# Performance work log

Measured on AMD Instinct MI355X. Metric: run time of the kernel, lower is better.

Reference implementation:

```python
import jax, jax.numpy as jnp
import numpy as np

B = 131072
EPS = 1e-5

def _attn(x, Wq, Wk, Wv, Wo):
    # x: (B, 10, 1); Wq/Wk/Wv: (1, 16); Wo: (16, 1)
    Q = x @ Wq  # (B, 10, 16)
    K = x @ Wk
    V = x @ Wv
    A = jnp.einsum('bqd,bkd->bqk', Q, K) / 4.0  # sqrt(16) = 4
    A = jax.nn.softmax(A, axis=1)  # NOTE: torch Softmax(dim=1) -> axis 1, not -1
    out = jnp.einsum('bqk,bkd->bqd', A, V) @ Wo  # (B, 10, 1)
    return out[..., 0]  # squeeze -> (B, 10)

def _bn(h, gamma, beta):
    # BatchNorm1d training-mode math (batch stats, biased variance)
    mu = jnp.mean(h, axis=0)
    var = jnp.mean(jnp.square(h - mu), axis=0)
    return gamma * (h - mu) * jax.lax.rsqrt(var + EPS) + beta

def setup_inputs() -> dict:
    key = jax.random.key(0)
    ks = jax.random.split(key, 24)
    n = lambda k, shp, s=1.0: (jax.random.normal(k, shp, dtype=jnp.float32) * s)
    inp = {
        'x':   n(ks[0], (B, 10, 1)),
        'Wq1': n(ks[1], (1, 16)), 'Wk1': n(ks[2], (1, 16)),
        'Wv1': n(ks[3], (1, 16)), 'Wo1': n(ks[4], (16, 1)),
        'Wq2': n(ks[5], (1, 16)), 'Wk2': n(ks[6], (1, 16)),
        'Wv2': n(ks[7], (1, 16)), 'Wo2': n(ks[8], (16, 1)),
        # layer1: Linear(10,128) BN ReLU Linear(128,256) BN ReLU Linear(256,10)
        'W1a': n(ks[9], (10, 128), 0.3), 'b1a': jnp.zeros((128,), jnp.float32),
        'g1a': jnp.ones((128,), jnp.float32), 'be1a': jnp.zeros((128,), jnp.float32),
        'W1b': n(ks[10], (128, 256), 0.09), 'b1b': jnp.zeros((256,), jnp.float32),
        'g1b': jnp.ones((256,), jnp.float32), 'be1b': jnp.zeros((256,), jnp.float32),
        'W1c': n(ks[11], (256, 10), 0.06), 'b1c': jnp.zeros((10,), jnp.float32),
        # layer2: Linear(10,128) BN ReLU Linear(128,256) BN ReLU Linear(256,2)
        'W2a': n(ks[12], (10, 128), 0.3), 'b2a': jnp.zeros((128,), jnp.float32),
        'g2a': jnp.ones((128,), jnp.float32), 'be2a': jnp.zeros((128,), jnp.float32),
        'W2b': n(ks[13], (128, 256), 0.09), 'b2b': jnp.zeros((256,), jnp.float32),
        'g2b': jnp.ones((256,), jnp.float32), 'be2b': jnp.zeros((256,), jnp.float32),
        'W2c': n(ks[14], (256, 2), 0.06), 'b2c': jnp.zeros((2,), jnp.float32),
    }
    return inp

def reference(x, Wq1, Wk1, Wv1, Wo1, Wq2, Wk2, Wv2, Wo2,
              W1a, b1a, g1a, be1a, W1b, b1b, g1b, be1b, W1c, b1c,
              W2a, b2a, g2a, be2a, W2b, b2b, g2b, be2b, W2c, b2c):
    h = _attn(x, Wq1, Wk1, Wv1, Wo1)                 # (B, 10)
    h = jax.nn.relu(_bn(h @ W1a + b1a, g1a, be1a))   # (B, 128)
    h = jax.nn.relu(_bn(h @ W1b + b1b, g1b, be1b))   # (B, 256)
    h = h @ W1c + b1c                                # (B, 10)
    h = _attn(h[..., None], Wq2, Wk2, Wv2, Wo2)      # (B, 10)
    h = jax.nn.relu(_bn(h @ W2a + b2a, g2a, be2a))   # (B, 128)
    h = jax.nn.relu(_bn(h @ W2b + b2b, g2b, be2b))   # (B, 256)
    return h @ W2c + b2c                             # (B, 2)
```

## Files before the change

### kernel.cpp

```cpp
#include <hip/hip_runtime.h>
#include <hip/hip_bf16.h>

#define EPS 1e-5f
constexpr int BN = 131072;
constexpr int NBKT = 32;

typedef __attribute__((ext_vector_type(8))) short bf16x8;
typedef __attribute__((ext_vector_type(4))) float f32x4;

constexpr size_t OFF_H   = 0;
constexpr size_t OFF_HH  = OFF_H  + (size_t)BN*10;
constexpr size_t OFF_M1  = OFF_HH + (size_t)BN*10;
constexpr size_t OFF_S2  = OFF_M1 + 65;
constexpr size_t OFF_M3  = OFF_S2 + 512;
constexpr size_t OFF_S4  = OFF_M3 + 65;
constexpr size_t OFF_WA1 = OFF_S4 + 512;
constexpr size_t OFF_BA1 = OFF_WA1 + 1280;
constexpr size_t OFF_WA2 = OFF_BA1 + 128;
constexpr size_t OFF_BA2 = OFF_WA2 + 1280;
constexpr size_t OFF_SC2 = OFF_BA2 + 128;
constexpr size_t OFF_TC2 = OFF_SC2 + 256;
constexpr size_t OFF_SC4 = OFF_TC2 + 256;
constexpr size_t OFF_TC4 = OFF_SC4 + 256;
constexpr size_t OFF_WB1 = OFF_TC4 + 256;
constexpr size_t OFF_BB1 = OFF_WB1 + 32768;
constexpr size_t OFF_WB2 = OFF_BB1 + 256;
constexpr size_t OFF_BB2 = OFF_WB2 + 32768;
constexpr size_t OFF_P1  = OFF_BB2 + 256;
constexpr size_t OFF_P3  = OFF_P1 + 1024*65;
constexpr size_t OFF_S2B = OFF_P3 + 1024*65;
constexpr size_t OFF_S4B = OFF_S2B + (size_t)NBKT*512;
constexpr size_t OFF_WT1 = OFF_S4B + (size_t)NBKT*512;
constexpr size_t OFF_WT2 = OFF_WT1 + 16384;
constexpr size_t OFF_END = OFF_WT2 + 16384;
constexpr size_t OFF_Z_BYTES = ((OFF_END*4 + 255) & ~(size_t)255);
constexpr size_t WS_NEED = OFF_Z_BYTES + (size_t)256*BN*2;

__device__ __forceinline__ float wsum(float v){
  v += __shfl_down(v, 32);
  v += __shfl_down(v, 16);
  v += __shfl_down(v, 8);
  v += __shfl_down(v, 4);
  v += __shfl_down(v, 2);
  v += __shfl_down(v, 1);
  return v;
}

__device__ __forceinline__ unsigned pk_bf16(float a, float b){
  union { __hip_bfloat16 h[2]; unsigned u; } cv;
  cv.h[0] = __float2bfloat16(a);
  cv.h[1] = __float2bfloat16(b);
  return cv.u;
}

__device__ __forceinline__ unsigned short bf16_1(float a){
  union { __hip_bfloat16 h; unsigned short u; } cv;
  cv.h = __float2bfloat16(a);
  return cv.u;
}

__device__ __forceinline__ void attn10(const float* xr, float cqk, float cvo, float* y){
  #pragma unroll
  for (int q=0;q<10;q++) y[q] = 0.f;
  #pragma unroll
  for (int k=0;k<10;k++){
    float t = cqk * xr[k];
    float m = t*xr[0];
    #pragma unroll
    for (int q=1;q<10;q++) m = fmaxf(m, t*xr[q]);
    float ex[10]; float s = 0.f;
    #pragma unroll
    for (int q=0;q<10;q++){ ex[q] = __expf(t*xr[q]-m); s += ex[q]; }
    float f = xr[k]/s;
    #pragma unroll
    for (int q=0;q<10;q++) y[q] += ex[q]*f;
  }
  #pragma unroll
  for (int q=0;q<10;q++) y[q] *= cvo;
}

__device__ __forceinline__ void moments_block(const float* y, float (*red)[65],
                                              float* Pb, int t, float scale){
  int lane = t & 63, w = t >> 6;
  #pragma unroll
  for (int i=0;i<10;i++){
    float v = wsum(y[i]);
    if (lane==0) red[w][i] = v;
  }
  #pragma unroll
  for (int i=0;i<10;i++){
    #pragma unroll
    for (int j=i;j<10;j++){
      float v = wsum(y[i]*y[j]);
      if (lane==0) red[w][10 + 10*i - i*(i-1)/2 + (j-i)] = v;
    }
  }
  __syncthreads();
  if (t < 65)
    Pb[(size_t)blockIdx.x*65 + t] = (red[0][t]+red[1][t]+red[2][t]+red[3][t])*scale;
}

__device__ __forceinline__ void moments10(const float* y, float* M, int lane){
  #pragma unroll
  for (int i=0;i<10;i++){
    float s = wsum(y[i]);
    if (lane==0) atomicAdd(&M[i], s);
  }
  #pragma unroll
  for (int i=0;i<10;i++){
    #pragma unroll
    for (int j=i;j<10;j++){
      int id = 10*i - i*(i-1)/2 + (j-i);
      float s = wsum(y[i]*y[j]);
      if (lane==0) atomicAdd(&M[10+id], s);
    }
  }
}

__global__ __launch_bounds__(256) void k_attn_in(
    const float* __restrict__ x,
    const float* __restrict__ Wq, const float* __restrict__ Wk,
    const float* __restrict__ Wv, const float* __restrict__ Wo,
    float* __restrict__ h, float* __restrict__ Pb){
  __shared__ float xs[256][11];
  __shared__ float red[4][65];
  int t = threadIdx.x;
  size_t base = (size_t)blockIdx.x*2560;
  for (int idx=t; idx<2560; idx+=256) xs[idx/10][idx%10] = x[base+idx];
  float cqk=0.f, cvo=0.f;
  #pragma unroll
  for (int d=0;d<16;d++){ cqk += Wq[d]*Wk[d]; cvo += Wv[d]*Wo[d]; }
  cqk *= 0.25f;
  __syncthreads();
  float xr[10];
  #pragma unroll
  for (int q=0;q<10;q++) xr[q] = xs[t][q];
  float y[10];
  attn10(xr, cqk, cvo, y);
  #pragma unroll
  for (int q=0;q<10;q++) xs[t][q] = y[q];
  moments_block(y, red, Pb, t, 1.0f);
  for (int idx=t; idx<2560; idx+=256) h[base+idx] = xs[idx/10][idx%10];
}

__global__ void k_fold10_part(const float* __restrict__ Pb, int npart,
                              const float* __restrict__ W,
                              const float* __restrict__ bv, const float* __restrict__ g,
                              const float* __restrict__ be,
                              float* __restrict__ WT, float* __restrict__ bo){
  __shared__ float part[65][8];
  __shared__ float sM[65];
  int t = threadIdx.x;
  if (t < 520){
    int c = t>>3, k = t&7;
    int n = npart>>3;
    float acc = 0.f;
    #pragma unroll 4
    for (int i=0;i<n;i++) acc += Pb[(size_t)(k*n+i)*65 + c];
    part[c][k] = acc;
  }
  __syncthreads();
  if (t < 65){
    float a = 0.f;
    #pragma unroll
    for (int k=0;k<8;k++) a += part[t][k];
    sM[t] = a;
  }
  __syncthreads();
  int j = t;
  if (j >= 128) return;
  const float invB = 1.f/(float)BN;
  float Eh[10];
  #pragma unroll
  for (int i=0;i<10;i++) Eh[i] = sM[i]*invB;
  float wj[10];
  #pragma unroll
  for (int i=0;i<10;i++) wj[i] = W[i*128+j];
  float mu = bv[j];
  #pragma unroll
  for (int i=0;i<10;i++) mu += Eh[i]*wj[i];
  float var = 0.f;
  #pragma unroll
  for (int i=0;i<10;i++){
    #pragma unroll
    for (int l=0;l<10;l++){
      int a = i<l ? i : l, c = i<l ? l : i;
      int id = 10*a - a*(a-1)/2 + (c-a);
      float cov = sM[10+id]*invB - Eh[i]*Eh[l];
      var += wj[i]*wj[l]*cov;
    }
  }
  float s = g[j]*rsqrtf(var + EPS);
  #pragma unroll
  for (int i=0;i<10;i++) WT[j*10+i] = wj[i]*s;
  bo[j] = (bv[j]-mu)*s + be[j];
}

__global__ void k_fold10_atomic(const float* __restrict__ M,
                                const float* __restrict__ W,
                                const float* __restrict__ bv, const float* __restrict__ g,
                                const float* __restrict__ be,
                                float* __restrict__ WT, float* __restrict__ bo){
  int j = threadIdx.x;
  if (j >= 128) return;
  const float invB = 1.f/(float)BN;
  float Eh[10];
  #pragma unroll
  for (int i=0;i<10;i++) Eh[i] = M[i]*invB;
  float wj[10];
  #pragma unroll
  for (int i=0;i<10;i++) wj[i] = W[i*128+j];
  float mu = bv[j];
  #pragma unroll
  for (int i=0;i<10;i++) mu += Eh[i]*wj[i];
  float var = 0.f;
  #pragma unroll
  for (int i=0;i<10;i++){
    #pragma unroll
    for (int l=0;l<10;l++){
      int a = i<l ? i : l, c = i<l ? l : i;
      int id = 10*a - a*(a-1)/2 + (c-a);
      float cov = M[10+id]*invB - Eh[i]*Eh[l];
      var += wj[i]*wj[l]*cov;
    }
  }
  float s = g[j]*rsqrtf(var + EPS);
  #pragma unroll
  for (int i=0;i<10;i++) WT[j*10+i] = wj[i]*s;
  bo[j] = (bv[j]-mu)*s + be[j];
}

__global__ void k_fold_affine(const float* __restrict__ stats,
                              const float* __restrict__ g,
                              const float* __restrict__ be,
                              float* __restrict__ s, float* __restrict__ tt){
  int j = threadIdx.x;
  if (j >= 256) return;
  float su = 0.f, sq = 0.f;
  #pragma unroll 4
  for (int k=0;k<NBKT;k++){
    su += stats[k*512 + j];
    sq += stats[k*512 + 256 + j];
  }
  const float invB = 1.f/(float)BN;
  float mu  = su*invB;
  float var = sq*invB - mu*mu;
  float sc = g[j]*rsqrtf(var + EPS);
  s[j]  = sc;
  tt[j] = be[j] - mu*sc;
}

__global__ __launch_bounds__(256) void k_prep_wt2(
    const float* __restrict__ W1, const float* __restrict__ W2,
    unsigned short* __restrict__ WT1, unsigned short* __restrict__ WT2){
  int g = blockIdx.x;
  const float* W = (g < 128) ? W1 : W2;
  unsigned short* WT = (g < 128) ? WT1 : WT2;
  int idx = (g & 127)*256 + threadIdx.x;
  int c = idx >> 7, k = idx & 127;
  WT[idx] = bf16_1(W[k*256 + c]);
}

__global__ __launch_bounds__(256) void k_layer_mfma(
    const float* __restrict__ h,
    const float* __restrict__ WaT,
    const float* __restrict__ ba,
    const unsigned short* __restrict__ WT,
    const float* __restrict__ bb,
    unsigned short* __restrict__ zt,
    float* __restrict__ stats)
{
  __shared__ unsigned short zs[256*72];
  __shared__ float hs[64][11];
  __shared__ float sWaT[1280];
  __shared__ float sstats[512];
  unsigned short* h1s = zs;
  int t = threadIdx.x;
  int lane = t & 63, w = t >> 6;
  int ci = lane & 15, g = lane >> 4;
  size_t row0 = (size_t)blockIdx.x * 64;

  bf16x8 bfr[4][4];
  #pragma unroll
  for (int nt=0; nt<4; nt++)
    #pragma unroll
    for (int kt=0; kt<4; kt++){
      union { uint4 u; bf16x8 v; } cv;
      cv.u = *(const uint4*)(WT + (size_t)(w*64 + nt*16 + ci)*128 + kt*32 + g*8);
      bfr[nt][kt] = cv.v;
    }

  for (int idx = t; idx < 640; idx += 256) hs[idx/10][idx%10] = h[row0*10 + idx];
  for (int idx = t; idx < 1280; idx += 256) sWaT[idx] = WaT[idx];
  __syncthreads();

  {
    int r = lane;
    int i0 = w * 32;
    float hr[10];
    #pragma unroll
    for (int l=0;l<10;l++) hr[l] = hs[r][l];
    #pragma unroll
    for (int j=0;j<4;j++){
      unsigned pk[4];
      #pragma unroll
      for (int q=0;q<4;q++){
        int i = i0 + j*8 + q*2;
        float v0 = ba[i], v1 = ba[i+1];
        #pragma unroll
        for (int l=0;l<10;l++){
          v0 = fmaf(hr[l], sWaT[i*10+l],     v0);
          v1 = fmaf(hr[l], sWaT[(i+1)*10+l], v1);
        }
        pk[q] = pk_bf16(fmaxf(v0,0.f), fmaxf(v1,0.f));
      }
      int byte = r*256 + (((i0 + j*8)*2) ^ ((r&7)<<4));
      *(uint4*)((char*)h1s + byte) = make_uint4(pk[0],pk[1],pk[2],pk[3]);
    }
  }
  __syncthreads();

  f32x4 acc[4][4];
  #pragma unroll
  for (int mt=0;mt<4;mt++)
    #pragma unroll
    for (int nt=0;nt<4;nt++)
      acc[mt][nt] = (f32x4){0.f,0.f,0.f,0.f};

  #pragma unroll
  for (int mt=0; mt<4; mt++){
    int r = mt*16 + ci;
    bf16x8 af[4];
    #pragma unroll
    for (int kt=0; kt<4; kt++){
      int byte = r*256 + ((kt*64 + g*16) ^ ((r&7)<<4));
      af[kt] = *(const bf16x8*)((const char*)h1s + byte);
    }
    #pragma unroll
    for (int nt=0; nt<4; nt++)
      #pragma unroll
      for (int kt=0; kt<4; kt++)
        acc[mt][nt] = __builtin_amdgcn_mfma_f32_16x16x32_bf16(
            af[kt], bfr[nt][kt], acc[mt][nt], 0, 0, 0);
  }

  float bbv[4];
  #pragma unroll
  for (int nt=0;nt<4;nt++) bbv[nt] = bb[w*64 + nt*16 + ci];
  float csum[4] = {0,0,0,0}, csq[4] = {0,0,0,0};
  #pragma unroll
  for (int mt=0; mt<4; mt++)
    #pragma unroll
    for (int nt=0; nt<4; nt++)
      #pragma unroll
      for (int j=0;j<4;j++){
        float zv = acc[mt][nt][j] + bbv[nt];
        acc[mt][nt][j] = zv;
        csum[nt] += zv;
        csq[nt]  += zv*zv;
      }
  #pragma unroll
  for (int nt=0; nt<4; nt++){
    float s1 = csum[nt], s2 = csq[nt];
    s1 += __shfl_down(s1, 32); s1 += __shfl_down(s1, 16);
    s2 += __shfl_down(s2, 32); s2 += __shfl_down(s2, 16);
    if (lane < 16){
      sstats[w*64 + nt*16 + ci]       = s1;
      sstats[256 + w*64 + nt*16 + ci] = s2;
    }
  }
  __syncthreads();
  int bkt = blockIdx.x & (NBKT-1);
  atomicAdd(&stats[bkt*512 + t], sstats[t]);
  atomicAdd(&stats[bkt*512 + 256 + t], sstats[256+t]);

  #pragma unroll
  for (int mt=0; mt<4; mt++)
    #pragma unroll
    for (int nt=0; nt<4; nt++){
      int c = w*64 + nt*16 + ci;
      int r0 = mt*16 + g*4;
      uint2 v;
      v.x = pk_bf16(acc[mt][nt][0], acc[mt][nt][1]);
      v.y = pk_bf16(acc[mt][nt][2], acc[mt][nt][3]);
      *(uint2*)&zs[c*72 + r0] = v;
    }
  __syncthreads();

  #pragma unroll
  for (int pass=0; pass<8; pass++){
    int c  = (t>>3) + pass*32;
    int rc = (t&7)*8;
    uint4 v = *(const uint4*)&zs[c*72 + rc];
    *(uint4*)(zt + (size_t)c*BN + row0 + rc) = v;
  }
}

__global__ __launch_bounds__(256) void k_consume_mid(
    const unsigned short* __restrict__ zt,
    const float* __restrict__ s_g, const float* __restrict__ t_g,
    const float* __restrict__ Wc,  const float* __restrict__ bc,
    const float* __restrict__ Wq, const float* __restrict__ Wk,
    const float* __restrict__ Wv, const float* __restrict__ Wo,
    float* __restrict__ hh, float* __restrict__ Pb){
  __shared__ float sW[2560];
  __shared__ float ss[256], st[256];
  __shared__ float red[4][65];
  __shared__ float hhs[128][11];
  int t = threadIdx.x;
  for (int idx=t; idx<2560; idx+=256) sW[idx] = Wc[idx];
  ss[t] = s_g[t]; st[t] = t_g[t];
  __syncthreads();
  int r = t >> 1, p = t & 1;
  size_t b = (size_t)blockIdx.x*128 + r;
  float z3[10];
  #pragma unroll
  for (int l=0;l<10;l++) z3[l] = p ? 0.f : bc[l];
  int c0 = p*128;
  #pragma unroll 4
  for (int c=c0; c<c0+128; c++){
    unsigned short u = zt[(size_t)c*BN + b];
    float f = __uint_as_float(((unsigned)u) << 16);
    float h2 = fmaxf(fmaf(ss[c], f, st[c]), 0.f);
    #pragma unroll
    for (int l=0;l<10;l++) z3[l] = fmaf(h2, sW[c*10+l], z3[l]);
  }
  #pragma unroll
  for (int l=0;l<10;l++) z3[l] += __shfl_xor(z3[l], 1);
  float cqk=0.f, cvo=0.f;
  #pragma unroll
  for (int d=0;d<16;d++){ cqk += Wq[d]*Wk[d]; cvo += Wv[d]*Wo[d]; }
  cqk *= 0.25f;
  float y[10];
  attn10(z3, cqk, cvo, y);
  if (!p){
    #pragma unroll
    for (int q=0;q<10;q++) hhs[r][q] = y[q];
  }
  moments_block(y, red, Pb, t, 0.5f);
  for (int idx=t; idx<1280; idx+=256)
    hh[(size_t)blockIdx.x*1280 + idx] = hhs[idx/10][idx%10];
}

__global__ __launch_bounds__(256) void k_consume_out(
    const unsigned short* __restrict__ zt,
    const float* __restrict__ s_g, const float* __restrict__ t_g,
    const float* __restrict__ Wc,  const float* __restrict__ bc,
    float* __restrict__ out){
  __shared__ float sW0[256], sW1[256], ss[256], st[256];
  int t = threadIdx.x;
  sW0[t] = Wc[t*2]; sW1[t] = Wc[t*2+1];
  ss[t] = s_g[t]; st[t] = t_g[t];
  __syncthreads();
  int r = t >> 1, p = t & 1;
  size_t b = (size_t)blockIdx.x*128 + r;
  float o0 = p ? 0.f : bc[0];
  float o1 = p ? 0.f : bc[1];
  int c0 = p*128;
  #pragma unroll 4
  for (int c=c0; c<c0+128; c++){
    unsigned short u = zt[(size_t)c*BN + b];
    float f = __uint_as_float(((unsigned)u) << 16);
    float h5 = fmaxf(fmaf(ss[c], f, st[c]), 0.f);
    o0 = fmaf(h5, sW0[c], o0);
    o1 = fmaf(h5, sW1[c], o1);
  }
  o0 += __shfl_xor(o0, 1);
  o1 += __shfl_xor(o1, 1);
  out[b*2 + p] = p ? o1 : o0;
}

__global__ void k_fold_big(const float* __restrict__ stats,
                           const float* __restrict__ W,
                           const float* __restrict__ bv, const float* __restrict__ g,
                           const float* __restrict__ be,
                           float* __restrict__ Wf, float* __restrict__ bf){
  int j = blockIdx.x*256 + threadIdx.x;
  if (j >= 256) return;
  const float invB = 1.f/(float)BN;
  float mu  = stats[j]*invB;
  float var = stats[256+j]*invB - mu*mu;
  float s = g[j]*rsqrtf(var + EPS);
  bf[j] = (bv[j]-mu)*s + be[j];
  for (int i=0;i<128;i++) Wf[i*256+j] = W[i*256+j]*s;
}

__global__ __launch_bounds__(256) void k_mid(
    const float* __restrict__ h,
    const float* __restrict__ WaT, const float* __restrict__ ba,
    const float* __restrict__ Wb,  const float* __restrict__ bb,
    float* __restrict__ stats){
  int b = blockIdx.x*256 + threadIdx.x;
  if (b >= BN) return;
  float hr[10];
  #pragma unroll
  for (int l=0;l<10;l++) hr[l] = h[(size_t)b*10+l];
  int lane = threadIdx.x & 63;
  for (int jc=0;jc<4;jc++){
    float acc[64];
    #pragma unroll
    for (int j=0;j<64;j++) acc[j] = bb[jc*64+j];
    for (int i=0;i<128;i++){
      float h1 = ba[i];
      #pragma unroll
      for (int l=0;l<10;l++) h1 += hr[l]*WaT[i*10+l];
      h1 = fmaxf(h1, 0.f);
      const float* __restrict__ w = &Wb[i*256 + jc*64];
      #pragma unroll
      for (int j=0;j<64;j++) acc[j] += h1*w[j];
    }
    #pragma unroll
    for (int j=0;j<64;j++){
      float s1 = wsum(acc[j]);
      float s2 = wsum(acc[j]*acc[j]);
      if (lane==0){
        atomicAdd(&stats[jc*64+j], s1);
        atomicAdd(&stats[256+jc*64+j], s2);
      }
    }
  }
}

__global__ __launch_bounds__(256) void k_mid2(
    const float* __restrict__ h,
    const float* __restrict__ WaT, const float* __restrict__ ba,
    const float* __restrict__ Wbf, const float* __restrict__ bbf,
    const float* __restrict__ Wc,  const float* __restrict__ bc,
    const float* __restrict__ Wq, const float* __restrict__ Wk,
    const float* __restrict__ Wv, const float* __restrict__ Wo,
    float* __restrict__ hh, float* __restrict__ M){
  int b = blockIdx.x*256 + threadIdx.x;
  if (b >= BN) return;
  float hr[10];
  #pragma unroll
  for (int l=0;l<10;l++) hr[l] = h[(size_t)b*10+l];
  float z3[10];
  #pragma unroll
  for (int l=0;l<10;l++) z3[l] = bc[l];
  for (int jc=0;jc<4;jc++){
    float acc[64];
    #pragma unroll
    for (int j=0;j<64;j++) acc[j] = bbf[jc*64+j];
    for (int i=0;i<128;i++){
      float h1 = ba[i];
      #pragma unroll
      for (int l=0;l<10;l++) h1 += hr[l]*WaT[i*10+l];
      h1 = fmaxf(h1, 0.f);
      const float* __restrict__ w = &Wbf[i*256 + jc*64];
      #pragma unroll
      for (int j=0;j<64;j++) acc[j] += h1*w[j];
    }
    #pragma unroll
    for (int j=0;j<64;j++){
      float h2 = fmaxf(acc[j], 0.f);
      const float* __restrict__ wc = &Wc[(jc*64+j)*10];
      #pragma unroll
      for (int l=0;l<10;l++) z3[l] += h2*wc[l];
    }
  }
  float cqk=0.f, cvo=0.f;
  #pragma unroll
  for (int d=0;d<16;d++){ cqk += Wq[d]*Wk[d]; cvo += Wv[d]*Wo[d]; }
  cqk *= 0.25f;
  float y[10];
  attn10(z3, cqk, cvo, y);
  #pragma unroll
  for (int q=0;q<10;q++) hh[(size_t)b*10+q] = y[q];
  moments10(y, M, threadIdx.x & 63);
}

__global__ __launch_bounds__(256) void k_out(
    const float* __restrict__ h,
    const float* __restrict__ WaT, const float* __restrict__ ba,
    const float* __restrict__ Wbf, const float* __restrict__ bbf,
    const float* __restrict__ Wc,  const float* __restrict__ bc,
    float* __restrict__ out){
  int b = blockIdx.x*256 + threadIdx.x;
  if (b >= BN) return;
  float hr[10];
  #pragma unroll
  for (int l=0;l<10;l++) hr[l] = h[(size_t)b*10+l];
  float o0 = bc[0], o1 = bc[1];
  for (int jc=0;jc<4;jc++){
    float acc[64];
    #pragma unroll
    for (int j=0;j<64;j++) acc[j] = bbf[jc*64+j];
    for (int i=0;i<128;i++){
      float h4 = ba[i];
      #pragma unroll
      for (int l=0;l<10;l++) h4 += hr[l]*WaT[i*10+l];
      h4 = fmaxf(h4, 0.f);
      const float* __restrict__ w = &Wbf[i*256 + jc*64];
      #pragma unroll
      for (int j=0;j<64;j++) acc[j] += h4*w[j];
    }
    #pragma unroll
    for (int j=0;j<64;j++){
      float h5 = fmaxf(acc[j], 0.f);
      o0 += h5*Wc[(jc*64+j)*2];
      o1 += h5*Wc[(jc*64+j)*2+1];
    }
  }
  out[(size_t)b*2]   = o0;
  out[(size_t)b*2+1] = o1;
}

extern "C" void kernel_launch(void* const* d_in, const int* in_sizes, int n_in,
                              void* d_out, int out_size, void* d_ws, size_t ws_size,
                              hipStream_t stream){
  const float* x   = (const float*)d_in[0];
  const float* Wq1 = (const float*)d_in[1];
  const float* Wk1 = (const float*)d_in[2];
  const float* Wv1 = (const float*)d_in[3];
  const float* Wo1 = (const float*)d_in[4];
  const float* Wq2 = (const float*)d_in[5];
  const float* Wk2 = (const float*)d_in[6];
  const float* Wv2 = (const float*)d_in[7];
  const float* Wo2 = (const float*)d_in[8];
  const float* W1a = (const float*)d_in[9];  const float* b1a = (const float*)d_in[10];
  const float* g1a = (const float*)d_in[11]; const float* be1a= (const float*)d_in[12];
  const float* W1b = (const float*)d_in[13]; const float* b1b = (const float*)d_in[14];
  const float* g1b = (const float*)d_in[15]; const float* be1b= (const float*)d_in[16];
  const float* W1c = (const float*)d_in[17]; const float* b1c = (const float*)d_in[18];
  const float* W2a = (const float*)d_in[19]; const float* b2a = (const float*)d_in[20];
  const float* g2a = (const float*)d_in[21]; const float* be2a= (const float*)d_in[22];
  const float* W2b = (const float*)d_in[23]; const float* b2b = (const float*)d_in[24];
  const float* g2b = (const float*)d_in[25]; const float* be2b= (const float*)d_in[26];
  const float* W2c = (const float*)d_in[27]; const float* b2c = (const float*)d_in[28];

  float* f   = (float*)d_ws;
  float* h   = f + OFF_H;
  float* hh  = f + OFF_HH;
  float* M1  = f + OFF_M1;
  float* S2  = f + OFF_S2;
  float* M3  = f + OFF_M3;
  float* S4  = f + OFF_S4;
  float* WA1 = f + OFF_WA1; float* BA1 = f + OFF_BA1;
  float* WA2 = f + OFF_WA2; float* BA2 = f + OFF_BA2;
  float* SC2 = f + OFF_SC2; float* TC2 = f + OFF_TC2;
  float* SC4 = f + OFF_SC4; float* TC4 = f + OFF_TC4;
  float* WB1 = f + OFF_WB1; float* BB1 = f + OFF_BB1;
  float* WB2 = f + OFF_WB2; float* BB2 = f + OFF_BB2;
  float* P1  = f + OFF_P1;  float* P3  = f + OFF_P3;
  float* S2B = f + OFF_S2B; float* S4B = f + OFF_S4B;
  unsigned short* WT1 = (unsigned short*)(f + OFF_WT1);
  unsigned short* WT2 = (unsigned short*)(f + OFF_WT2);
  unsigned short* ZT = (unsigned short*)((char*)d_ws + OFF_Z_BYTES);

  dim3 blk(256);
  dim3 grid256(BN/256);
  dim3 grid128(BN/128);
  dim3 grid64(BN/64);

  if (ws_size >= WS_NEED){
    hipMemsetAsync(S2B, 0, (size_t)2*NBKT*512*sizeof(float), stream);
    k_prep_wt2<<<256,blk,0,stream>>>(W1b, W2b, WT1, WT2);
    k_attn_in<<<grid256,blk,0,stream>>>(x, Wq1,Wk1,Wv1,Wo1, h, P1);
    k_fold10_part<<<1,576,0,stream>>>(P1, 512, W1a,b1a,g1a,be1a, WA1,BA1);
    k_layer_mfma<<<grid64,blk,0,stream>>>(h, WA1,BA1, WT1,b1b, ZT, S2B);
    k_fold_affine<<<1,256,0,stream>>>(S2B, g1b, be1b, SC2, TC2);
    k_consume_mid<<<grid128,blk,0,stream>>>(ZT, SC2,TC2, W1c,b1c,
                                            Wq2,Wk2,Wv2,Wo2, hh, P3);
    k_fold10_part<<<1,576,0,stream>>>(P3, 1024, W2a,b2a,g2a,be2a, WA2,BA2);
    k_layer_mfma<<<grid64,blk,0,stream>>>(hh, WA2,BA2, WT2,b2b, ZT, S4B);
    k_fold_affine<<<1,256,0,stream>>>(S4B, g2b, be2b, SC4, TC4);
    k_consume_out<<<grid128,blk,0,stream>>>(ZT, SC4,TC4, W2c,b2c, (float*)d_out);
  } else {
    hipMemsetAsync(M1, 0, (65+512+65+512)*sizeof(float), stream);
    k_attn_in<<<grid256,blk,0,stream>>>(x, Wq1,Wk1,Wv1,Wo1, h, P1);
    k_fold10_part<<<1,576,0,stream>>>(P1, 512, W1a,b1a,g1a,be1a, WA1,BA1);
    k_mid<<<grid256,blk,0,stream>>>(h, WA1,BA1, W1b,b1b, S2);
    k_fold_big<<<1,256,0,stream>>>(S2, W1b,b1b,g1b,be1b, WB1,BB1);
    k_mid2<<<grid256,blk,0,stream>>>(h, WA1,BA1, WB1,BB1, W1c,b1c,
                                     Wq2,Wk2,Wv2,Wo2, hh, M3);
    k_fold10_atomic<<<1,128,0,stream>>>(M3, W2a,b2a,g2a,be2a, WA2,BA2);
    k_mid<<<grid256,blk,0,stream>>>(hh, WA2,BA2, W2b,b2b, S4);
    k_fold_big<<<1,256,0,stream>>>(S4, W2b,b2b,g2b,be2b, WB2,BB2);
    k_out<<<grid256,blk,0,stream>>>(hh, WA2,BA2, WB2,BB2, W2c,b2c, (float*)d_out);
  }
}
```

Measured before the change: 228.9 us.

## Stage transposed bf16 activations through LDS with wide loads in consumer kernels

The two consumer kernels now process 256 rows per block with one thread per row, instead of two threads per row splitting the channels. Each block stages 64-channel chunks of the column-major bf16 activation buffer into shared memory using 16-byte vector loads, then reads them per thread. This replaces the narrow 2-byte strided global loads and the cross-lane shuffle reduction. The block count halves, the partial-moment count passed to the fold kernel changes from 1024 to 512, and the 0.5 scale factor is dropped. The extra syncthreads per chunk and 32KB of LDS may reduce occupancy.

```diff
diff --git a/kernel.cpp b/kernel.cpp
--- a/kernel.cpp
+++ b/kernel.cpp
@@ -80,7 +80,7 @@
 }
 
 __device__ __forceinline__ void moments_block(const float* y, float (*red)[65],
-                                              float* Pb, int t, float scale){
+                                              float* Pb, int t){
   int lane = t & 63, w = t >> 6;
   #pragma unroll
   for (int i=0;i<10;i++){
@@ -97,7 +97,7 @@
   }
   __syncthreads();
   if (t < 65)
-    Pb[(size_t)blockIdx.x*65 + t] = (red[0][t]+red[1][t]+red[2][t]+red[3][t])*scale;
+    Pb[(size_t)blockIdx.x*65 + t] = red[0][t]+red[1][t]+red[2][t]+red[3][t];
 }
 
 __device__ __forceinline__ void moments10(const float* y, float* M, int lane){
@@ -139,7 +139,7 @@
   attn10(xr, cqk, cvo, y);
   #pragma unroll
   for (int q=0;q<10;q++) xs[t][q] = y[q];
-  moments_block(y, red, Pb, t, 1.0f);
+  moments_block(y, red, Pb, t);
   for (int idx=t; idx<2560; idx+=256) h[base+idx] = xs[idx/10][idx%10];
 }
 
@@ -403,43 +403,53 @@
     const float* __restrict__ Wq, const float* __restrict__ Wk,
     const float* __restrict__ Wv, const float* __restrict__ Wo,
     float* __restrict__ hh, float* __restrict__ Pb){
+  __shared__ __align__(16) unsigned short zs[64*256];
   __shared__ float sW[2560];
   __shared__ float ss[256], st[256];
   __shared__ float red[4][65];
-  __shared__ float hhs[128][11];
   int t = threadIdx.x;
   for (int idx=t; idx<2560; idx+=256) sW[idx] = Wc[idx];
   ss[t] = s_g[t]; st[t] = t_g[t];
-  __syncthreads();
-  int r = t >> 1, p = t & 1;
-  size_t b = (size_t)blockIdx.x*128 + r;
+  size_t b0 = (size_t)blockIdx.x*256;
+
   float z3[10];
   #pragma unroll
-  for (int l=0;l<10;l++) z3[l] = p ? 0.f : bc[l];
-  int c0 = p*128;
-  #pragma unroll 4
-  for (int c=c0; c<c0+128; c++){
-    unsigned short u = zt[(size_t)c*BN + b];
-    float f = __uint_as_float(((unsigned)u) << 16);
-    float h2 = fmaxf(fmaf(ss[c], f, st[c]), 0.f);
-    #pragma unroll
-    for (int l=0;l<10;l++) z3[l] = fmaf(h2, sW[c*10+l], z3[l]);
-  }
-  #pragma unroll
-  for (int l=0;l<10;l++) z3[l] += __shfl_xor(z3[l], 1);
+  for (int l=0;l<10;l++) z3[l] = bc[l];
+
+  int lane32 = t & 31, cl8 = t >> 5;
+  for (int cc=0; cc<4; cc++){
+    __syncthreads();
+    #pragma unroll
+    for (int pass=0; pass<8; pass++){
+      int c_local = pass*8 + cl8;
+      int c = cc*64 + c_local;
+      uint4 v = *(const uint4*)(zt + (size_t)c*BN + b0 + lane32*8);
+      *(uint4*)&zs[c_local*256 + lane32*8] = v;
+    }
+    __syncthreads();
+    #pragma unroll 8
+    for (int c_local=0; c_local<64; c_local++){
+      int c = cc*64 + c_local;
+      float f = __uint_as_float(((unsigned)zs[c_local*256 + t]) << 16);
+      float h2 = fmaxf(fmaf(ss[c], f, st[c]), 0.f);
+      #pragma unroll
+      for (int l=0;l<10;l++) z3[l] = fmaf(h2, sW[c*10+l], z3[l]);
+    }
+  }
+
   float cqk=0.f, cvo=0.f;
   #pragma unroll
   for (int d=0;d<16;d++){ cqk += Wq[d]*Wk[d]; cvo += Wv[d]*Wo[d]; }
   cqk *= 0.25f;
   float y[10];
   attn10(z3, cqk, cvo, y);
-  if (!p){
-    #pragma unroll
-    for (int q=0;q<10;q++) hhs[r][q] = y[q];
-  }
-  moments_block(y, red, Pb, t, 0.5f);
-  for (int idx=t; idx<1280; idx+=256)
-    hh[(size_t)blockIdx.x*1280 + idx] = hhs[idx/10][idx%10];
+  __syncthreads();
+  float* hhs = (float*)zs;
+  #pragma unroll
+  for (int q=0;q<10;q++) hhs[t*10+q] = y[q];
+  moments_block(y, red, Pb, t);
+  for (int idx=t; idx<2560; idx+=256)
+    hh[b0*10 + idx] = hhs[idx];
 }
 
 __global__ __launch_bounds__(256) void k_consume_out(
@@ -447,27 +457,34 @@
     const float* __restrict__ s_g, const float* __restrict__ t_g,
     const float* __restrict__ Wc,  const float* __restrict__ bc,
     float* __restrict__ out){
+  __shared__ __align__(16) unsigned short zs[64*256];
   __shared__ float sW0[256], sW1[256], ss[256], st[256];
   int t = threadIdx.x;
   sW0[t] = Wc[t*2]; sW1[t] = Wc[t*2+1];
   ss[t] = s_g[t]; st[t] = t_g[t];
-  __syncthreads();
-  int r = t >> 1, p = t & 1;
-  size_t b = (size_t)blockIdx.x*128 + r;
-  float o0 = p ? 0.f : bc[0];
-  float o1 = p ? 0.f : bc[1];
-  int c0 = p*128;
-  #pragma unroll 4
-  for (int c=c0; c<c0+128; c++){
-    unsigned short u = zt[(size_t)c*BN + b];
-    float f = __uint_as_float(((unsigned)u) << 16);
-    float h5 = fmaxf(fmaf(ss[c], f, st[c]), 0.f);
-    o0 = fmaf(h5, sW0[c], o0);
-    o1 = fmaf(h5, sW1[c], o1);
-  }
-  o0 += __shfl_xor(o0, 1);
-  o1 += __shfl_xor(o1, 1);
-  out[b*2 + p] = p ? o1 : o0;
+  size_t b0 = (size_t)blockIdx.x*256;
+  float o0 = bc[0], o1 = bc[1];
+  int lane32 = t & 31, cl8 = t >> 5;
+  for (int cc=0; cc<4; cc++){
+    __syncthreads();
+    #pragma unroll
+    for (int pass=0; pass<8; pass++){
+      int c_local = pass*8 + cl8;
+      int c = cc*64 + c_local;
+      uint4 v = *(const uint4*)(zt + (size_t)c*BN + b0 + lane32*8);
+      *(uint4*)&zs[c_local*256 + lane32*8] = v;
+    }
+    __syncthreads();
+    #pragma unroll 8
+    for (int c_local=0; c_local<64; c_local++){
+      int c = cc*64 + c_local;
+      float f = __uint_as_float(((unsigned)zs[c_local*256 + t]) << 16);
+      float h5 = fmaxf(fmaf(ss[c], f, st[c]), 0.f);
+      o0 = fmaf(h5, sW0[c], o0);
+      o1 = fmaf(h5, sW1[c], o1);
+    }
+  }
+  *(float2*)(out + (b0 + t)*2) = make_float2(o0, o1);
 }
 
 __global__ void k_fold_big(const float* __restrict__ stats,
@@ -649,7 +666,6 @@
 
   dim3 blk(256);
   dim3 grid256(BN/256);
-  dim3 grid128(BN/128);
   dim3 grid64(BN/64);
 
   if (ws_size >= WS_NEED){
@@ -659,12 +675,12 @@
     k_fold10_part<<<1,576,0,stream>>>(P1, 512, W1a,b1a,g1a,be1a, WA1,BA1);
     k_layer_mfma<<<grid64,blk,0,stream>>>(h, WA1,BA1, WT1,b1b, ZT, S2B);
     k_fold_affine<<<1,256,0,stream>>>(S2B, g1b, be1b, SC2, TC2);
-    k_consume_mid<<<grid128,blk,0,stream>>>(ZT, SC2,TC2, W1c,b1c,
+    k_consume_mid<<<grid256,blk,0,stream>>>(ZT, SC2,TC2, W1c,b1c,
                                             Wq2,Wk2,Wv2,Wo2, hh, P3);
-    k_fold10_part<<<1,576,0,stream>>>(P3, 1024, W2a,b2a,g2a,be2a, WA2,BA2);
+    k_fold10_part<<<1,576,0,stream>>>(P3, 512, W2a,b2a,g2a,be2a, WA2,BA2);
     k_layer_mfma<<<grid64,blk,0,stream>>>(hh, WA2,BA2, WT2,b2b, ZT, S4B);
     k_fold_affine<<<1,256,0,stream>>>(S4B, g2b, be2b, SC4, TC4);
-    k_consume_out<<<grid128,blk,0,stream>>>(ZT, SC4,TC4, W2c,b2c, (float*)d_out);
+    k_consume_out<<<grid256,blk,0,stream>>>(ZT, SC4,TC4, W2c,b2c, (float*)d_out);
   } else {
     hipMemsetAsync(M1, 0, (65+512+65+512)*sizeof(float), stream);
     k_attn_in<<<grid256,blk,0,stream>>>(x, Wq1,Wk1,Wv1,Wo1, h, P1);
```

Result: faster. 209.9 us (-8.3%).
